# Optimization experiments

Measured on AMD Instinct MI355X. Metric: run time of the kernel, lower is better.

Reference implementation:

```python
import jax, jax.numpy as jnp
import numpy as np

# Module constants (from init_kwargs)
B, NIN, NOUT = 128, 1024, 1024
G_OFF, G_ON, K_V = 0.001, 0.003, 0.5


def setup_inputs() -> dict:
    key = jax.random.key(0)
    k1, k2, k3 = jax.random.split(key, 3)
    stdv = 1.0 / np.sqrt(NIN)
    x = jax.random.normal(k1, (B, NIN), dtype=jnp.float32)
    # NonNeg-constrained weights, RandomNormal(mean=0.5, std=1/sqrt(in))
    w_pos = jnp.abs(0.5 + stdv * jax.random.normal(k2, (NIN, NOUT), dtype=jnp.float32))
    w_neg = jnp.abs(0.5 + stdv * jax.random.normal(k3, (NIN, NOUT), dtype=jnp.float32))
    b_pos = jnp.full((NOUT,), 0.5, dtype=jnp.float32)
    b_neg = jnp.full((NOUT,), 0.5, dtype=jnp.float32)
    return {"x": x, "w_pos": w_pos, "w_neg": w_neg, "b_pos": b_pos, "b_neg": b_neg}


def reference(x, w_pos, w_neg, b_pos, b_neg):
    # combine_weights(): append bias row, interleave pos/neg columns -> [in+1, 2*out]
    comb_pos = jnp.concatenate([w_pos, b_pos[None, :]], axis=0)  # [in+1, out]
    comb_neg = jnp.concatenate([w_neg, b_neg[None, :]], axis=0)  # [in+1, out]
    weights = jnp.stack([comb_pos, comb_neg], axis=-1).reshape(NIN + 1, 2 * NOUT)

    # append ones column for bias input; scale to voltages
    ones = jnp.ones((x.shape[0], 1), dtype=x.dtype)
    voltages = K_V * jnp.concatenate([x, ones], axis=1)  # [B, in+1]

    # double_weights_to_conductances: linear map of weights into [G_off, G_on]
    max_w = jnp.max(weights)
    k_cond = (G_ON - G_OFF) / max_w
    conductances = k_cond * weights + G_OFF  # [in+1, 2*out]

    # eval path: expand-multiply-reduce == matmul (same math, fused here)
    currents = voltages @ conductances  # [B, 2*out]

    # differential pair readout and rescale back to weight units
    total_currents = currents[:, 0::2] - currents[:, 1::2]  # [B, out]
    y_disturbed = total_currents / (K_V * k_cond)
    return y_disturbed
```

## Files before the change

### kernel.cpp

```cpp
#include <hip/hip_runtime.h>


#define NB   128
#define NIN  1024
#define NOUT 1024

#define OT   64
#define KC   32
#define NKS  (NIN / KC)
#define XS   132
#define WDS  68

__device__ __forceinline__ unsigned short f32_to_bf16_rne(float f) {
    union { float f; unsigned u; } c; c.f = f;
    unsigned u = c.u + 0x7FFFu + ((c.u >> 16) & 1u);
    return (unsigned short)(u >> 16);
}
__device__ __forceinline__ float bf16_to_f32(unsigned short h) {
    union { unsigned u; float f; } c; c.u = ((unsigned)h) << 16;
    return c.f;
}

__global__ __launch_bounds__(128) void memr_partial(
    const float* __restrict__ x,  const float* __restrict__ wp,
    const float* __restrict__ wn, unsigned short* __restrict__ ws)
{
    __shared__ float xs[KC * XS];
    __shared__ float wd[KC * WDS];

    const int t  = threadIdx.x;
    const int o0 = blockIdx.x * OT;
    const int ks = blockIdx.y;
    const int k0 = ks * KC;

    #pragma unroll
    for (int r = 0; r < 8; ++r) {
        const int f4 = r * 128 + t;
        const int b  = f4 >> 3;
        const int q  = f4 & 7;
        const float4 v = *(const float4*)&x[(size_t)b * NIN + k0 + q * 4];
        xs[(q * 4 + 0) * XS + b] = v.x;
        xs[(q * 4 + 1) * XS + b] = v.y;
        xs[(q * 4 + 2) * XS + b] = v.z;
        xs[(q * 4 + 3) * XS + b] = v.w;
    }
    #pragma unroll
    for (int r = 0; r < 4; ++r) {
        const int f4 = r * 128 + t;
        const int kk = f4 >> 4;
        const int q  = f4 & 15;
        const size_t g = (size_t)(k0 + kk) * NOUT + o0 + q * 4;
        const float4 p = *(const float4*)&wp[g];
        const float4 n = *(const float4*)&wn[g];
        float4 d;
        d.x = p.x - n.x; d.y = p.y - n.y; d.z = p.z - n.z; d.w = p.w - n.w;
        *(float4*)&wd[kk * WDS + q * 4] = d;
    }
    __syncthreads();

    const int to = t & 7;
    const int tb = t >> 3;

    float acc[8][8];
    #pragma unroll
    for (int i = 0; i < 8; ++i)
        #pragma unroll
        for (int j = 0; j < 8; ++j) acc[i][j] = 0.f;

    const float* xr = &xs[tb * 8];
    const float* wr = &wd[to * 8];

    #pragma unroll 4
    for (int kk = 0; kk < KC; ++kk) {
        const float4 xa = *(const float4*)&xr[kk * XS];
        const float4 xb = *(const float4*)&xr[kk * XS + 4];
        const float4 wa = *(const float4*)&wr[kk * WDS];
        const float4 wb = *(const float4*)&wr[kk * WDS + 4];
        const float xv[8] = {xa.x, xa.y, xa.z, xa.w, xb.x, xb.y, xb.z, xb.w};
        const float wv[8] = {wa.x, wa.y, wa.z, wa.w, wb.x, wb.y, wb.z, wb.w};
        #pragma unroll
        for (int i = 0; i < 8; ++i)
            #pragma unroll
            for (int j = 0; j < 8; ++j)
                acc[i][j] += xv[i] * wv[j];
    }

    unsigned short* wsb = ws + (size_t)ks * NB * NOUT + o0 + to * 8;
    #pragma unroll
    for (int i = 0; i < 8; ++i) {
        const int b = tb * 8 + i;
        ushort4 v0, v1;
        v0.x = f32_to_bf16_rne(acc[i][0]); v0.y = f32_to_bf16_rne(acc[i][1]);
        v0.z = f32_to_bf16_rne(acc[i][2]); v0.w = f32_to_bf16_rne(acc[i][3]);
        v1.x = f32_to_bf16_rne(acc[i][4]); v1.y = f32_to_bf16_rne(acc[i][5]);
        v1.z = f32_to_bf16_rne(acc[i][6]); v1.w = f32_to_bf16_rne(acc[i][7]);
        *(ushort4*)&wsb[(size_t)b * NOUT]     = v0;
        *(ushort4*)&wsb[(size_t)b * NOUT + 4] = v1;
    }
}

__global__ __launch_bounds__(256) void memr_reduce(
    const unsigned short* __restrict__ ws, const float* __restrict__ bp,
    const float* __restrict__ bn, float* __restrict__ out)
{
    const int g  = blockIdx.x * 256 + threadIdx.x;
    const int i4 = g * 4;
    const int o4 = i4 & (NOUT - 1);

    const float4 bpv = *(const float4*)&bp[o4];
    const float4 bnv = *(const float4*)&bn[o4];
    float s0 = bpv.x - bnv.x, s1 = bpv.y - bnv.y;
    float s2 = bpv.z - bnv.z, s3 = bpv.w - bnv.w;

    #pragma unroll
    for (int ks = 0; ks < NKS; ++ks) {
        const ushort4 u = *(const ushort4*)&ws[(size_t)ks * NB * NOUT + i4];
        s0 += bf16_to_f32(u.x); s1 += bf16_to_f32(u.y);
        s2 += bf16_to_f32(u.z); s3 += bf16_to_f32(u.w);
    }
    float4 o; o.x = s0; o.y = s1; o.z = s2; o.w = s3;
    *(float4*)&out[i4] = o;
}

extern "C" void kernel_launch(void* const* d_in, const int* in_sizes, int n_in,
                              void* d_out, int out_size, void* d_ws, size_t ws_size,
                              hipStream_t stream)
{
    const float* x  = (const float*)d_in[0];
    const float* wp = (const float*)d_in[1];
    const float* wn = (const float*)d_in[2];
    const float* bp = (const float*)d_in[3];
    const float* bn = (const float*)d_in[4];
    float* out = (float*)d_out;
    unsigned short* ws = (unsigned short*)d_ws;

    dim3 g1(NOUT / OT, NKS);
    memr_partial<<<g1, 128, 0, stream>>>(x, wp, wn, ws);
    memr_reduce<<<NB * NOUT / 4 / 256, 256, 0, stream>>>(ws, bp, bn, out);
}
```

Baseline: 78.57 us.

## Load weight differences directly from global into registers with double buffering

Removes the shared-memory staging of the w_pos minus w_neg tile. Each thread now reads its 8 weight columns per k straight from global memory into registers, with a two-stage register prefetch that overlaps the next row's load with the current FMA block. This saves LDS space and one barrier's worth of staging. In exchange, each weight element is reloaded by all 16 batch-group threads through cache rather than shared, and the subtraction is repeated per thread.

Result: slower. 82.11 us (+4.5%).

```diff
diff --git a/kernel.cpp b/kernel.cpp
--- a/kernel.cpp
+++ b/kernel.cpp
@@ -9,7 +9,6 @@
 #define KC   32
 #define NKS  (NIN / KC)
 #define XS   132
-#define WDS  68
 
 __device__ __forceinline__ unsigned short f32_to_bf16_rne(float f) {
     union { float f; unsigned u; } c; c.f = f;
@@ -26,7 +25,6 @@
     const float* __restrict__ wn, unsigned short* __restrict__ ws)
 {
     __shared__ float xs[KC * XS];
-    __shared__ float wd[KC * WDS];
 
     const int t  = threadIdx.x;
     const int o0 = blockIdx.x * OT;
@@ -44,22 +42,14 @@
         xs[(q * 4 + 2) * XS + b] = v.z;
         xs[(q * 4 + 3) * XS + b] = v.w;
     }
-    #pragma unroll
-    for (int r = 0; r < 4; ++r) {
-        const int f4 = r * 128 + t;
-        const int kk = f4 >> 4;
-        const int q  = f4 & 15;
-        const size_t g = (size_t)(k0 + kk) * NOUT + o0 + q * 4;
-        const float4 p = *(const float4*)&wp[g];
-        const float4 n = *(const float4*)&wn[g];
-        float4 d;
-        d.x = p.x - n.x; d.y = p.y - n.y; d.z = p.z - n.z; d.w = p.w - n.w;
-        *(float4*)&wd[kk * WDS + q * 4] = d;
-    }
     __syncthreads();
 
     const int to = t & 7;
     const int tb = t >> 3;
+
+    const float* xr  = &xs[tb * 8];
+    const float* wpr = wp + (size_t)k0 * NOUT + o0 + to * 8;
+    const float* wnr = wn + (size_t)k0 * NOUT + o0 + to * 8;
 
     float acc[8][8];
     #pragma unroll
@@ -67,22 +57,52 @@
         #pragma unroll
         for (int j = 0; j < 8; ++j) acc[i][j] = 0.f;
 
-    const float* xr = &xs[tb * 8];
-    const float* wr = &wd[to * 8];
+    float4 Apa = *(const float4*)&wpr[0];
+    float4 Apb = *(const float4*)&wpr[4];
+    float4 Ana = *(const float4*)&wnr[0];
+    float4 Anb = *(const float4*)&wnr[4];
 
-    #pragma unroll 4
-    for (int kk = 0; kk < KC; ++kk) {
-        const float4 xa = *(const float4*)&xr[kk * XS];
-        const float4 xb = *(const float4*)&xr[kk * XS + 4];
-        const float4 wa = *(const float4*)&wr[kk * WDS];
-        const float4 wb = *(const float4*)&wr[kk * WDS + 4];
-        const float xv[8] = {xa.x, xa.y, xa.z, xa.w, xb.x, xb.y, xb.z, xb.w};
-        const float wv[8] = {wa.x, wa.y, wa.z, wa.w, wb.x, wb.y, wb.z, wb.w};
-        #pragma unroll
-        for (int i = 0; i < 8; ++i)
+    #pragma unroll 2
+    for (int kk = 0; kk < KC; kk += 2) {
+        const size_t ofB = (size_t)(kk + 1) * NOUT;
+        float4 Bpa = *(const float4*)&wpr[ofB];
+        float4 Bpb = *(const float4*)&wpr[ofB + 4];
+        float4 Bna = *(const float4*)&wnr[ofB];
+        float4 Bnb = *(const float4*)&wnr[ofB + 4];
+
+        {
+            const float4 xa = *(const float4*)&xr[kk * XS];
+            const float4 xb = *(const float4*)&xr[kk * XS + 4];
+            const float xv[8] = {xa.x, xa.y, xa.z, xa.w, xb.x, xb.y, xb.z, xb.w};
+            const float wv[8] = {
+                Apa.x - Ana.x, Apa.y - Ana.y, Apa.z - Ana.z, Apa.w - Ana.w,
+                Apb.x - Anb.x, Apb.y - Anb.y, Apb.z - Anb.z, Apb.w - Anb.w};
             #pragma unroll
-            for (int j = 0; j < 8; ++j)
-                acc[i][j] += xv[i] * wv[j];
+            for (int i = 0; i < 8; ++i)
+                #pragma unroll
+                for (int j = 0; j < 8; ++j)
+                    acc[i][j] += xv[i] * wv[j];
+        }
+
+        const size_t ofA = (size_t)((kk + 2) & (KC - 1)) * NOUT;
+        Apa = *(const float4*)&wpr[ofA];
+        Apb = *(const float4*)&wpr[ofA + 4];
+        Ana = *(const float4*)&wnr[ofA];
+        Anb = *(const float4*)&wnr[ofA + 4];
+
+        {
+            const float4 xa = *(const float4*)&xr[(kk + 1) * XS];
+            const float4 xb = *(const float4*)&xr[(kk + 1) * XS + 4];
+            const float xv[8] = {xa.x, xa.y, xa.z, xa.w, xb.x, xb.y, xb.z, xb.w};
+            const float wv[8] = {
+                Bpa.x - Bna.x, Bpa.y - Bna.y, Bpa.z - Bna.z, Bpa.w - Bna.w,
+                Bpb.x - Bnb.x, Bpb.y - Bnb.y, Bpb.z - Bnb.z, Bpb.w - Bnb.w};
+            #pragma unroll
+            for (int i = 0; i < 8; ++i)
+                #pragma unroll
+                for (int j = 0; j < 8; ++j)
+                    acc[i][j] += xv[i] * wv[j];
+        }
     }
 
     unsigned short* wsb = ws + (size_t)ks * NB * NOUT + o0 + to * 8;
```
